# Performance work log

Measured on AMD Instinct MI355X. Metric: run time of the kernel, lower is better.

Reference implementation:

```python
import jax, jax.numpy as jnp
import numpy as np
import math

H = 1024
B, S = 4, 2048

def setup_inputs() -> dict:
    key = jax.random.key(0)
    k0, k1, k2, k3, k4 = jax.random.split(key, 5)
    scale = 1.0 / math.sqrt(H)
    return {
        "input_seq_rep": jax.random.normal(k0, (B, S, H), dtype=jnp.float32),
        "Wk": jax.random.uniform(k1, (H, H), dtype=jnp.float32, minval=-scale, maxval=scale),
        "bk": jax.random.uniform(k2, (H,), dtype=jnp.float32, minval=-scale, maxval=scale),
        "Wq": jax.random.uniform(k3, (H, H), dtype=jnp.float32, minval=-scale, maxval=scale),
        "bq": jax.random.uniform(k4, (H,), dtype=jnp.float32, minval=-scale, maxval=scale),
        "k_mul": 64,
    }

def reference(input_seq_rep, Wk, bk, Wq, bq, k_mul):
    b, s, h = input_seq_rep.shape
    x = jax.nn.relu(input_seq_rep)
    # torch Linear: x @ W.T + b
    k = jnp.einsum('bsh,oh->bso', x, Wk) + bk   # key (also used as value)
    q = jnp.einsum('bsh,oh->bso', x, Wq) + bq
    scores = jnp.einsum('bqh,bkh->bqk', q, k) / jnp.sqrt(jnp.float32(h))
    # Faithful mask: banded window only for batch index 0; other batches all-zero mask
    i = jnp.arange(s)[:, None]
    j = jnp.arange(s)[None, :]
    band = ((j <= i) & (j >= i - k_mul)).astype(jnp.float32)  # (S,S)
    mask = jnp.zeros((b, s, s), dtype=jnp.float32).at[0].set(band)
    scores = jnp.where(mask == 0, jnp.float32(-1e9), scores)
    p_attn = jax.nn.softmax(scores, axis=-1)
    out = jnp.einsum('bqk,bkh->bqh', p_attn, k)
    return out, p_attn
```

## Files before the change

kernel.cpp:

```cpp
#include <hip/hip_runtime.h>

#define SD 2048
#define HD 1024
#define BD 4

typedef __bf16 bf16_t;
typedef bf16_t bf16x8 __attribute__((ext_vector_type(8)));
typedef float f32x4 __attribute__((ext_vector_type(4)));
typedef unsigned short ushortx8 __attribute__((ext_vector_type(8)));
typedef unsigned short ushort_t;

__device__ inline unsigned short f2bf(float f) {
  return __builtin_bit_cast(unsigned short, (__bf16)f);
}

__device__ inline float bf2f(unsigned short u) {
  return __builtin_bit_cast(float, (unsigned)u << 16);
}

__device__ inline void gload_lds16(const void* g, void* l) {
  __builtin_amdgcn_global_load_lds(
      (const __attribute__((address_space(1))) void*)g,
      (__attribute__((address_space(3))) void*)l, 16, 0, 0);
}

template <int ROWS>
__device__ inline void stage_rows(const ushort_t* __restrict__ src, int r0, int k0,
                                  int tid, ushort_t* lds)
{
#pragma unroll
  for (int it = 0; it < ROWS / 32; ++it) {
    int c   = it * 256 + tid;
    int row = c >> 3;
    int kc8 = c & 7;
    int kcs = kc8 ^ (row & 7);
    gload_lds16(&src[(size_t)(r0 + row) * HD + k0 + kcs * 8], &lds[c * 8]);
  }
}

__device__ inline bf16x8 lds_frag(const ushort_t* l, int row, int kc8) {
  int kcs = kc8 ^ (row & 7);
  return *(const bf16x8*)&l[row * 64 + kcs * 8];
}

__global__ __launch_bounds__(256) void prep(
    const float* __restrict__ X, const float* __restrict__ Wk,
    const float* __restrict__ Wq, ushort_t* __restrict__ Xb,
    ushort_t* __restrict__ Wkb, ushort_t* __restrict__ Wqb)
{
  const int n8x = SD * HD / 8;
  const int n8w = HD * HD / 8;
  const int e = blockIdx.x * 256 + threadIdx.x;
  const float4* s4; ushortx8* d8; int idx; bool relu;
  if (e < n8x)            { s4 = (const float4*)X;  d8 = (ushortx8*)Xb;  idx = e;             relu = true; }
  else if (e < n8x + n8w) { s4 = (const float4*)Wk; d8 = (ushortx8*)Wkb; idx = e - n8x;       relu = false; }
  else                    { s4 = (const float4*)Wq; d8 = (ushortx8*)Wqb; idx = e - n8x - n8w; relu = false; }
  float4 a = s4[idx * 2], b4 = s4[idx * 2 + 1];
  float v[8] = {a.x, a.y, a.z, a.w, b4.x, b4.y, b4.z, b4.w};
  ushortx8 o;
#pragma unroll
  for (int j = 0; j < 8; ++j) {
    float f = v[j];
    if (relu) f = fmaxf(f, 0.0f);
    o[j] = f2bf(f);
  }
  d8[idx] = o;
}

__global__ __launch_bounds__(256, 2) void gemm_kq(
    const ushort_t* __restrict__ Xb, const ushort_t* __restrict__ Wkb,
    const ushort_t* __restrict__ Wqb, const float* __restrict__ bk,
    const float* __restrict__ bq, ushort_t* __restrict__ Kb,
    ushort_t* __restrict__ Qb, const float* __restrict__ X,
    float* __restrict__ part, float* __restrict__ P0)
{
  __shared__ __align__(16) ushort_t lA[2][8192];
  __shared__ __align__(16) ushort_t lB[2][8192];

  const int bid = blockIdx.x;
  const int tid = threadIdx.x;

  if (bid >= 352) {
    const int f = bid - 352;
    const int nf4 = SD * (SD / 4);
    float4 z = make_float4(0.f, 0.f, 0.f, 0.f);
    float4* p4 = (float4*)P0;
    for (int e = f * 256 + tid; e < nf4; e += 128 * 256) p4[e] = z;
    return;
  }
  if (bid >= 256) {
    const int cid = bid - 256;
    const int b = cid >> 5;
    const int sub = cid & 31;
    const float4* Xp = (const float4*)(X + (size_t)(b + 1) * SD * HD + (size_t)sub * 64 * HD);
    float4 acc = make_float4(0.f, 0.f, 0.f, 0.f);
#pragma unroll 4
    for (int rr = 0; rr < 64; ++rr) {
      float4 v = Xp[rr * 256 + tid];
      acc.x += fmaxf(v.x, 0.f); acc.y += fmaxf(v.y, 0.f);
      acc.z += fmaxf(v.z, 0.f); acc.w += fmaxf(v.w, 0.f);
    }
    ((float4*)part)[((size_t)b * 32 + sub) * 256 + tid] = acc;
    return;
  }

  const int wg = ((bid & 7) << 5) | (bid >> 3);
  const int bm = wg >> 4, bn = wg & 15;
  const int half = bn >> 3;
  const ushort_t* Bm = half ? Wqb : Wkb;
  const int m0 = bm * 128, n0 = (bn & 7) * 128;

  const int lane = tid & 63;
  const int wave = tid >> 6;
  const int wm = wave >> 1, wn = wave & 1;

  f32x4 acc[4][4] = {};

  stage_rows<128>(Xb, m0, 0, tid, lA[0]);
  stage_rows<128>(Bm, n0, 0, tid, lB[0]);
  __syncthreads();

  for (int t = 0; t < 16; ++t) {
    const int cur = t & 1;
    if (t < 15) {
      stage_rows<128>(Xb, m0, (t + 1) * 64, tid, lA[cur ^ 1]);
      stage_rows<128>(Bm, n0, (t + 1) * 64, tid, lB[cur ^ 1]);
    }
#pragma unroll
    for (int h = 0; h < 2; ++h) {
      bf16x8 af[4], bfr[4];
#pragma unroll
      for (int mi = 0; mi < 4; ++mi)
        af[mi] = lds_frag(lA[cur], wm * 64 + mi * 16 + (lane & 15), h * 4 + (lane >> 4));
#pragma unroll
      for (int ni = 0; ni < 4; ++ni)
        bfr[ni] = lds_frag(lB[cur], wn * 64 + ni * 16 + (lane & 15), h * 4 + (lane >> 4));
#pragma unroll
      for (int mi = 0; mi < 4; ++mi)
#pragma unroll
        for (int ni = 0; ni < 4; ++ni)
          acc[mi][ni] = __builtin_amdgcn_mfma_f32_16x16x32_bf16(af[mi], bfr[ni], acc[mi][ni], 0, 0, 0);
    }
    __syncthreads();
  }

  const int rb = (lane >> 4) * 4;
  const int cc = lane & 15;
  const float* bias = half ? bq : bk;
  ushort_t* dst = half ? Qb : Kb;
#pragma unroll
  for (int ni = 0; ni < 4; ++ni) {
    int col = n0 + wn * 64 + ni * 16 + cc;
    float bv = bias[col];
#pragma unroll
    for (int mi = 0; mi < 4; ++mi) {
#pragma unroll
      for (int j = 0; j < 4; ++j) {
        int row = m0 + wm * 64 + mi * 16 + rb + j;
        dst[(size_t)row * HD + col] = f2bf(acc[mi][ni][j] + bv);
      }
    }
  }
}

__global__ __launch_bounds__(256, 2) void band_cm(
    const ushort_t* __restrict__ Q, const ushort_t* __restrict__ K,
    float* __restrict__ Sb0, float* __restrict__ Sb1,
    const float* __restrict__ part, const float* __restrict__ Wk,
    const float* __restrict__ bk, float* __restrict__ cm,
    float* __restrict__ patRest)
{
  __shared__ __align__(16) char smem[32768];
  const int bid = blockIdx.x;
  const int tid = threadIdx.x;

  if (bid >= 174) {
    const int f = bid - 174;
    const int nf4 = 3 * SD * (SD / 4);
    const float uf = 1.0f / SD;
    float4 v = make_float4(uf, uf, uf, uf);
    float4* p4 = (float4*)patRest;
    for (int e = f * 256 + tid; e < nf4; e += 384 * 256) p4[e] = v;
    return;
  }

  if (bid < 126) {
    const int tt = bid >> 1;
    const int ks = bid & 1;
    const int blk = (tt + 1) >> 1;
    const int tcol = (tt + 1) & 1;
    const int m0 = blk * 64;
    const int n0 = (blk - 1 + tcol) * 64;
    float* Sb = ks ? Sb1 : Sb0;

    const int lane = tid & 63;
    const int wave = tid >> 6;
    const int wm = wave >> 1, wn = wave & 1;

    ushort_t* lA = (ushort_t*)smem;
    ushort_t* lB = (ushort_t*)(smem + 16384);

    f32x4 acc[2][2] = {};

    const int kbase = ks * 512;
    stage_rows<64>(Q, m0, kbase, tid, lA);
    stage_rows<64>(K, n0, kbase, tid, lB);
    __syncthreads();

    for (int t = 0; t < 8; ++t) {
      const int cur = t & 1;
      if (t < 7) {
        stage_rows<64>(Q, m0, kbase + (t + 1) * 64, tid, lA + (cur ^ 1) * 4096);
        stage_rows<64>(K, n0, kbase + (t + 1) * 64, tid, lB + (cur ^ 1) * 4096);
      }
#pragma unroll
      for (int h = 0; h < 2; ++h) {
        bf16x8 af[2], bfr[2];
#pragma unroll
        for (int mi = 0; mi < 2; ++mi)
          af[mi] = lds_frag(lA + cur * 4096, wm * 32 + mi * 16 + (lane & 15), h * 4 + (lane >> 4));
#pragma unroll
        for (int ni = 0; ni < 2; ++ni)
          bfr[ni] = lds_frag(lB + cur * 4096, wn * 32 + ni * 16 + (lane & 15), h * 4 + (lane >> 4));
#pragma unroll
        for (int mi = 0; mi < 2; ++mi)
#pragma unroll
          for (int ni = 0; ni < 2; ++ni)
            acc[mi][ni] = __builtin_amdgcn_mfma_f32_16x16x32_bf16(af[mi], bfr[ni], acc[mi][ni], 0, 0, 0);
      }
      __syncthreads();
    }

    const int rb = (lane >> 4) * 4;
    const int cc = lane & 15;
#pragma unroll
    for (int ni = 0; ni < 2; ++ni) {
      int ccol = tcol * 64 + wn * 32 + ni * 16 + cc;
#pragma unroll
      for (int mi = 0; mi < 2; ++mi)
#pragma unroll
        for (int j = 0; j < 4; ++j) {
          int row = m0 + wm * 32 + mi * 16 + rb + j;
          Sb[(size_t)row * 128 + ccol] = acc[mi][ni][j] * 0.03125f;
        }
    }
    return;
  }

  {
    const int cid = bid - 126;
    const int b = cid >> 4, og = cid & 15;
    float* xs = (float*)smem;
#pragma unroll
    for (int k = 0; k < 4; ++k) {
      int h = tid + 256 * k;
      float a = 0;
#pragma unroll 8
      for (int rc = 0; rc < 32; ++rc) a += part[((size_t)b * 32 + rc) * HD + h];
      xs[h] = a;
    }
    __syncthreads();
    const int o = og * 64 + (tid >> 2);
    const int q = tid & 3;
    const f32x4* wr = (const f32x4*)(Wk + (size_t)o * HD);
    const f32x4* x4 = (const f32x4*)xs;
    float a = 0;
#pragma unroll 8
    for (int i = 0; i < 64; ++i) {
      f32x4 w = wr[q * 64 + i], x = x4[q * 64 + i];
      a += w[0] * x[0] + w[1] * x[1] + w[2] * x[2] + w[3] * x[3];
    }
    a += __shfl_xor(a, 1);
    a += __shfl_xor(a, 2);
    if (q == 0) cm[b * HD + o] = a * (1.0f / SD) + bk[o];
  }
}

__global__ __launch_bounds__(256, 2) void pv_epi(
    const float* __restrict__ Sb0, const float* __restrict__ Sb1,
    const ushort_t* __restrict__ Kb, const float* __restrict__ cm,
    float* __restrict__ out0, float* __restrict__ P0,
    float* __restrict__ out123)
{
  __shared__ __align__(16) float smem[15488];
  const int bid = blockIdx.x;
  const int t = threadIdx.x;

  if (bid < 512) {
    float* Ks  = smem;
    float* spl = smem + 12288;
    const int i0 = (bid >> 3) * 32;
    const int hc = bid & 7;

    for (int e = t; e < 96 * 16; e += 256) {
      int lr = e >> 4, c8 = e & 15;
      int gr = i0 - 64 + lr;
      if (gr < 0) gr = 0;
      ushortx8 u = *(const ushortx8*)&Kb[(size_t)gr * HD + hc * 128 + c8 * 8];
      f32x4 f0 = {bf2f(u[0]), bf2f(u[1]), bf2f(u[2]), bf2f(u[3])};
      f32x4 f1 = {bf2f(u[4]), bf2f(u[5]), bf2f(u[6]), bf2f(u[7])};
      *(f32x4*)&Ks[lr * 128 + c8 * 8]     = f0;
      *(f32x4*)&Ks[lr * 128 + c8 * 8 + 4] = f1;
    }

    {
      const int r = t >> 3, sub = t & 7;
      const int i = i0 + r;
      const int jlo = (i >= 64) ? i - 64 : 0;
      const int scoff = i0 & 32;
      float sv[12];
      float m = -1e30f;
#pragma unroll
      for (int k = 0; k < 12; ++k) {
        int lj = sub + 8 * k;
        int gj = i0 - 64 + lj;
        bool val = (gj >= jlo) && (gj <= i);
        float s = -1e30f;
        if (val) {
          size_t sidx = (size_t)i * 128 + lj + scoff;
          s = Sb0[sidx] + Sb1[sidx];
        }
        sv[k] = s;
        m = fmaxf(m, s);
      }
#pragma unroll
      for (int off = 1; off < 8; off <<= 1) m = fmaxf(m, __shfl_xor(m, off));
      float p[12], sum = 0;
#pragma unroll
      for (int k = 0; k < 12; ++k) {
        p[k] = (sv[k] > -1e29f) ? __expf(sv[k] - m) : 0.0f;
        sum += p[k];
      }
#pragma unroll
      for (int off = 1; off < 8; off <<= 1) sum += __shfl_xor(sum, off);
      float inv = 1.0f / sum;
#pragma unroll
      for (int k = 0; k < 12; ++k) {
        int lj = sub + 8 * k;
        float pv = p[k] * inv;
        spl[r * 100 + lj] = pv;
        if (hc == 0 && sv[k] > -1e29f)
          P0[(size_t)i * SD + (i0 - 64 + lj)] = pv;
      }
    }
    __syncthreads();

    const int r = t >> 3;
    const int g = t & 7;
    f32x4 a0 = {0,0,0,0}, a1 = {0,0,0,0}, a2 = {0,0,0,0}, a3 = {0,0,0,0};
    for (int lj = 0; lj < 96; ++lj) {
      float pv = spl[r * 100 + lj];
      const float* kr = &Ks[lj * 128 + g * 4];
      a0 += pv * *(const f32x4*)(kr);
      a1 += pv * *(const f32x4*)(kr + 32);
      a2 += pv * *(const f32x4*)(kr + 64);
      a3 += pv * *(const f32x4*)(kr + 96);
    }
    float* ob = out0 + (size_t)(i0 + r) * HD + hc * 128 + g * 4;
    *(f32x4*)(ob)      = a0;
    *(f32x4*)(ob + 32) = a1;
    *(f32x4*)(ob + 64) = a2;
    *(f32x4*)(ob + 96) = a3;
    return;
  }

  {
    const int nf4 = 3 * SD * (HD / 4);
    const int per_b = SD * (HD / 4);
    const f32x4* cm4 = (const f32x4*)cm;
    f32x4* o4 = (f32x4*)out123;
    for (int idx = (bid - 512) * 256 + t; idx < nf4; idx += 512 * 256) {
      int b = idx / per_b;
      int h4 = idx & (HD / 4 - 1);
      o4[idx] = cm4[b * (HD / 4) + h4];
    }
  }
}

extern "C" void kernel_launch(void* const* d_in, const int* in_sizes, int n_in,
                              void* d_out, int out_size, void* d_ws, size_t ws_size,
                              hipStream_t stream)
{
  (void)in_sizes; (void)n_in; (void)out_size; (void)ws_size;
  const float* X  = (const float*)d_in[0];
  const float* Wk = (const float*)d_in[1];
  const float* bk = (const float*)d_in[2];
  const float* Wq = (const float*)d_in[3];
  const float* bq = (const float*)d_in[4];

  float* out = (float*)d_out;
  float* pat = out + (size_t)BD * SD * HD;

  char* w = (char*)d_ws;
  ushort_t* Xb   = (ushort_t*)w; w += (size_t)SD * HD * 2;
  ushort_t* Wkb  = (ushort_t*)w; w += (size_t)HD * HD * 2;
  ushort_t* Wqb  = (ushort_t*)w; w += (size_t)HD * HD * 2;
  ushort_t* Kb0  = (ushort_t*)w; w += (size_t)SD * HD * 2;
  ushort_t* Q0b  = (ushort_t*)w; w += (size_t)SD * HD * 2;
  float*    part = (float*)w;    w += (size_t)3 * 32 * HD * 4;
  float*    cm   = (float*)w;    w += (size_t)3 * HD * 4;
  float*    Sb0  = (float*)w;    w += (size_t)SD * 128 * 4;
  float*    Sb1  = (float*)w;    w += (size_t)SD * 128 * 4;

  prep<<<2048, 256, 0, stream>>>(X, Wk, Wq, Xb, Wkb, Wqb);
  gemm_kq<<<480, 256, 0, stream>>>(Xb, Wkb, Wqb, bk, bq, Kb0, Q0b, X, part, pat);
  band_cm<<<558, 256, 0, stream>>>(Q0b, Kb0, Sb0, Sb1, part, Wk, bk, cm,
                                   pat + (size_t)SD * SD);
  pv_epi<<<1024, 256, 0, stream>>>(Sb0, Sb1, Kb0, cm, out, pat, out + (size_t)SD * HD);
}
```

Measured before the change: 68.61 us.

## Fuse fp32-to-bf16 conversion and ReLU into GEMM staging, drop prep kernel

Removes the separate prep kernel that converted X, Wk and Wq to bf16. The GEMM now loads fp32 tiles from global memory into registers, overlaps those loads with the MFMA compute, and then converts (applying ReLU for X) and writes swizzled bf16 into LDS. This saves a kernel launch and the write and reread of the bf16 copies. In exchange it doubles the bytes the GEMM reads from global memory, drops the direct global-to-LDS loads, and raises register pressure by 16 f32x4 staging registers, which may hurt occupancy at two blocks per CU.

```diff
diff --git a/kernel.cpp b/kernel.cpp
--- a/kernel.cpp
+++ b/kernel.cpp
@@ -43,36 +43,47 @@
   return *(const bf16x8*)&l[row * 64 + kcs * 8];
 }
 
-__global__ __launch_bounds__(256) void prep(
+__device__ inline void stage_load(const float* __restrict__ src, int r0, int k0,
+                                  int tid, f32x4* regs)
+{
+#pragma unroll
+  for (int it = 0; it < 4; ++it) {
+    int c   = it * 256 + tid;
+    int row = c >> 3;
+    int kc8 = c & 7;
+    const float* g = &src[(size_t)(r0 + row) * HD + k0 + kc8 * 8];
+    regs[it * 2]     = *(const f32x4*)g;
+    regs[it * 2 + 1] = *(const f32x4*)(g + 4);
+  }
+}
+
+template <bool RELU>
+__device__ inline void stage_write(const f32x4* regs, int tid, ushort_t* lds)
+{
+#pragma unroll
+  for (int it = 0; it < 4; ++it) {
+    int c   = it * 256 + tid;
+    int row = c >> 3;
+    int kc8 = c & 7;
+    int kcs = kc8 ^ (row & 7);
+    f32x4 v0 = regs[it * 2], v1 = regs[it * 2 + 1];
+    ushortx8 o;
+#pragma unroll
+    for (int j = 0; j < 4; ++j) {
+      float f0 = v0[j], f1 = v1[j];
+      if (RELU) { f0 = fmaxf(f0, 0.f); f1 = fmaxf(f1, 0.f); }
+      o[j] = f2bf(f0); o[4 + j] = f2bf(f1);
+    }
+    *(ushortx8*)&lds[row * 64 + kcs * 8] = o;
+  }
+}
+
+__global__ __launch_bounds__(256, 2) void gemm_kq(
     const float* __restrict__ X, const float* __restrict__ Wk,
-    const float* __restrict__ Wq, ushort_t* __restrict__ Xb,
-    ushort_t* __restrict__ Wkb, ushort_t* __restrict__ Wqb)
-{
-  const int n8x = SD * HD / 8;
-  const int n8w = HD * HD / 8;
-  const int e = blockIdx.x * 256 + threadIdx.x;
-  const float4* s4; ushortx8* d8; int idx; bool relu;
-  if (e < n8x)            { s4 = (const float4*)X;  d8 = (ushortx8*)Xb;  idx = e;             relu = true; }
-  else if (e < n8x + n8w) { s4 = (const float4*)Wk; d8 = (ushortx8*)Wkb; idx = e - n8x;       relu = false; }
-  else                    { s4 = (const float4*)Wq; d8 = (ushortx8*)Wqb; idx = e - n8x - n8w; relu = false; }
-  float4 a = s4[idx * 2], b4 = s4[idx * 2 + 1];
-  float v[8] = {a.x, a.y, a.z, a.w, b4.x, b4.y, b4.z, b4.w};
-  ushortx8 o;
-#pragma unroll
-  for (int j = 0; j < 8; ++j) {
-    float f = v[j];
-    if (relu) f = fmaxf(f, 0.0f);
-    o[j] = f2bf(f);
-  }
-  d8[idx] = o;
-}
-
-__global__ __launch_bounds__(256, 2) void gemm_kq(
-    const ushort_t* __restrict__ Xb, const ushort_t* __restrict__ Wkb,
-    const ushort_t* __restrict__ Wqb, const float* __restrict__ bk,
+    const float* __restrict__ Wq, const float* __restrict__ bk,
     const float* __restrict__ bq, ushort_t* __restrict__ Kb,
-    ushort_t* __restrict__ Qb, const float* __restrict__ X,
-    float* __restrict__ part, float* __restrict__ P0)
+    ushort_t* __restrict__ Qb, float* __restrict__ part,
+    float* __restrict__ P0)
 {
   __shared__ __align__(16) ushort_t lA[2][8192];
   __shared__ __align__(16) ushort_t lB[2][8192];
@@ -107,7 +118,7 @@
   const int wg = ((bid & 7) << 5) | (bid >> 3);
   const int bm = wg >> 4, bn = wg & 15;
   const int half = bn >> 3;
-  const ushort_t* Bm = half ? Wqb : Wkb;
+  const float* Bsrc = half ? Wq : Wk;
   const int m0 = bm * 128, n0 = (bn & 7) * 128;
 
   const int lane = tid & 63;
@@ -115,16 +126,19 @@
   const int wm = wave >> 1, wn = wave & 1;
 
   f32x4 acc[4][4] = {};
-
-  stage_rows<128>(Xb, m0, 0, tid, lA[0]);
-  stage_rows<128>(Bm, n0, 0, tid, lB[0]);
+  f32x4 ra[8], rbv[8];
+
+  stage_load(X, m0, 0, tid, ra);
+  stage_load(Bsrc, n0, 0, tid, rbv);
+  stage_write<true>(ra, tid, lA[0]);
+  stage_write<false>(rbv, tid, lB[0]);
   __syncthreads();
 
   for (int t = 0; t < 16; ++t) {
     const int cur = t & 1;
     if (t < 15) {
-      stage_rows<128>(Xb, m0, (t + 1) * 64, tid, lA[cur ^ 1]);
-      stage_rows<128>(Bm, n0, (t + 1) * 64, tid, lB[cur ^ 1]);
+      stage_load(X, m0, (t + 1) * 64, tid, ra);
+      stage_load(Bsrc, n0, (t + 1) * 64, tid, rbv);
     }
 #pragma unroll
     for (int h = 0; h < 2; ++h) {
@@ -140,6 +154,10 @@
 #pragma unroll
         for (int ni = 0; ni < 4; ++ni)
           acc[mi][ni] = __builtin_amdgcn_mfma_f32_16x16x32_bf16(af[mi], bfr[ni], acc[mi][ni], 0, 0, 0);
+    }
+    if (t < 15) {
+      stage_write<true>(ra, tid, lA[cur ^ 1]);
+      stage_write<false>(rbv, tid, lB[cur ^ 1]);
     }
     __syncthreads();
   }
@@ -392,9 +410,6 @@
   float* pat = out + (size_t)BD * SD * HD;
 
   char* w = (char*)d_ws;
-  ushort_t* Xb   = (ushort_t*)w; w += (size_t)SD * HD * 2;
-  ushort_t* Wkb  = (ushort_t*)w; w += (size_t)HD * HD * 2;
-  ushort_t* Wqb  = (ushort_t*)w; w += (size_t)HD * HD * 2;
   ushort_t* Kb0  = (ushort_t*)w; w += (size_t)SD * HD * 2;
   ushort_t* Q0b  = (ushort_t*)w; w += (size_t)SD * HD * 2;
   float*    part = (float*)w;    w += (size_t)3 * 32 * HD * 4;
@@ -402,8 +417,7 @@
   float*    Sb0  = (float*)w;    w += (size_t)SD * 128 * 4;
   float*    Sb1  = (float*)w;    w += (size_t)SD * 128 * 4;
 
-  prep<<<2048, 256, 0, stream>>>(X, Wk, Wq, Xb, Wkb, Wqb);
-  gemm_kq<<<480, 256, 0, stream>>>(Xb, Wkb, Wqb, bk, bq, Kb0, Q0b, X, part, pat);
+  gemm_kq<<<480, 256, 0, stream>>>(X, Wk, Wq, bk, bq, Kb0, Q0b, part, pat);
   band_cm<<<558, 256, 0, stream>>>(Q0b, Kb0, Sb0, Sb1, part, Wk, bk, cm,
                                    pat + (size_t)SD * SD);
   pv_epi<<<1024, 256, 0, stream>>>(Sb0, Sb1, Kb0, cm, out, pat, out + (size_t)SD * HD);
```

Result: slower. 71.24 us (+3.8%).
